# Kernel optimization log

Measured on AMD Instinct MI355X. Metric: run time of the kernel, lower is better.

## Reference

```python
import jax, jax.numpy as jnp
import numpy as np

B, D, NN = 16, 2, 100        # batch, num_depots, num_nodes (pickups+deliveries)
N2 = NN // 2                 # pickups (= deliveries)
NA = D + NN                  # total nodes per batch graph
H, HE, L = 128, 64, 3        # hidden_node_dim, hidden_edge_dim, conv_layers
SLOPE, EPS = 0.2, 1e-5


def _bn(x, g, b):
    # BatchNorm1d in training mode: per-feature batch stats (biased var)
    m = jnp.mean(x, axis=0)
    v = jnp.var(x, axis=0)
    return (x - m) * jax.lax.rsqrt(v + EPS) * g + b


def _leaky(x):
    return jnp.where(x >= 0, x, SLOPE * x)


def _prop(xk, e, m, Wg):
    # Dense-equivalent of GatConv.propagate over a fully-connected per-batch grid.
    # Edge (i, j): x_i = x[target j], x_j = x[source i] (matches edge_index layout:
    # row0 = i repeated, row1 = j blockwise; PyG target = edge_index[1]).
    # xk: [B, N, H] transformed node feats; e: [B, N, N, HE]; m: [B, N, N] 0/1.
    h = xk.shape[-1]
    wi, wj, we = Wg[:h], Wg[h:2 * h], Wg[2 * h:]  # split cat([x_i, x_j, e]) @ Wg
    alpha = _leaky((xk @ wi)[:, None, :, :]        # x_i contribution (target j)
                   + (xk @ wj)[:, :, None, :]      # x_j contribution (source i)
                   + jnp.einsum('bijc,ch->bijh', e, we))
    alpha = jnp.where(m[..., None] != 0, alpha, -jnp.inf)
    alpha = jax.nn.softmax(alpha, axis=1)          # segment softmax keyed by target j
    return jnp.einsum('bijh,bih->bjh', alpha, xk)  # scatter-add x_j * alpha to targets


def _forward(x, demand, time_window, edge_attr_d, edge_attr_r,
             W0, W1, W2, W3, W4,
             b0_g, b0_b, b1_g, b1_b, b2_g, b2_b, b3_g, b3_b, b4_g, b4_b,
             ff_w1, ff_b1, ff_w2, ff_b2, bn_g, bn_b,
             Wvla, Wvlp, Wvld, Wga, Wgp, Wgd,
             edge_index, mask_adjacency_d, mask_adjacency_r):
    ds = jnp.concatenate([x, demand, time_window], axis=-1)  # [B, NA, 5]
    dep = _bn(ds[:, :D].reshape(B * D, -1) @ W0, b0_g, b0_b).reshape(B, D, H)
    pk_in = jnp.concatenate([ds[:, D:D + N2], ds[:, D + N2:D + NN]], axis=-1).reshape(B * N2, -1)
    pk = _bn(pk_in @ W1, b1_g, b1_b).reshape(B, N2, H)
    dl = _bn(ds[:, D + N2:D + NN].reshape(B * N2, -1) @ W2, b2_g, b2_b).reshape(B, N2, H)
    e_d = _bn(edge_attr_d.reshape(-1, edge_attr_d.shape[-1]) @ W3, b3_g, b3_b).reshape(B, NA, NA, HE)
    e_r = _bn(edge_attr_r.reshape(-1, edge_attr_r.shape[-1]) @ W4, b4_g, b4_b).reshape(B, NA, NA, HE)
    m_d = mask_adjacency_d.reshape(B, NA, NA)
    m_r = mask_adjacency_r.reshape(B, NA, NA)

    def conv(xc, e, m, l):
        xall = xc @ Wvla[l]
        pick = xc[:, D:D + N2] @ Wvlp[l]
        deli = xc[:, D + N2:D + NN] @ Wvld[l]
        X1 = _prop(xall, e, m, Wga[l])
        X2 = _prop(pick, e[:, D:D + N2, D:D + N2], m[:, D:D + N2, D:D + N2], Wgp[l])
        X3 = _prop(deli, e[:, D + N2:D + NN, D + N2:D + NN], m[:, D + N2:D + NN, D + N2:D + NN], Wgd[l])
        # faithful to torch.cat(dim=0) followed by view(B, -1, H)
        Xc = jnp.concatenate([X1.reshape(-1, H), X2.reshape(-1, H), X3.reshape(-1, H)], axis=0).reshape(B, -1, H)
        xa, xp, xdd = Xc[:, :NA], Xc[:, NA:NA + N2], Xc[:, NA + N2:NA + NN]
        return jnp.concatenate([xa[:, :D], xa[:, D:D + N2] + xp, xa[:, D + N2:] + xdd], axis=1)

    xd = jnp.concatenate([dep, pk, dl], axis=1)  # [B, NA, H]
    xr = xd
    for l in range(L):
        xd, xr = conv(xd, e_d, m_d, l), conv(xr, e_r, m_r, l)

    def ff_bn(xc):
        xf = xc.reshape(-1, H)
        f = jax.nn.relu(xf @ ff_w1 + ff_b1) @ ff_w2 + ff_b2
        return _bn(xf + f, bn_g, bn_b).reshape(B, NA, H)

    return ff_bn(xd), ff_bn(xr)


def setup_inputs() -> dict:
    key = jax.random.key(0)
    it = iter(jax.random.split(key, 40))

    def nrm(shape, s=0.05):
        return (s * jax.random.normal(next(it), shape)).astype(jnp.float32)

    def uni(shape):
        return jax.random.uniform(next(it), shape, dtype=jnp.float32)

    x = nrm((B, NA, 2), 1.0)
    # first D entries per batch are depots (demand == 0), rest are nonzero
    demand = jnp.concatenate([jnp.zeros((B, D, 1), jnp.float32), uni((B, NN, 1)) + 0.5], axis=1)
    time_window = uni((B, NA, 2))
    edge_attr_d = uni((B, NA * NA, 2))
    edge_attr_r = uni((B, NA * NA, 2))
    eye = jnp.eye(NA, dtype=jnp.int32)[None]
    mask_d = jnp.maximum(jax.random.randint(next(it), (B, NA, NA), 0, 2, dtype=jnp.int32), eye).reshape(B, NA * NA)
    mask_r = jnp.maximum(jax.random.randint(next(it), (B, NA, NA), 0, 2, dtype=jnp.int32), eye).reshape(B, NA * NA)
    ii = jnp.arange(B * NA, dtype=jnp.int32)
    edge_index = jnp.stack([jnp.repeat(ii, NA), jnp.repeat(ii.reshape(B, NA), NA, axis=0).reshape(-1)])

    inp = dict(
        x=x, demand=demand, time_window=time_window,
        edge_attr_d=edge_attr_d, edge_attr_r=edge_attr_r,
        W0=nrm((5, H)), W1=nrm((10, H)), W2=nrm((5, H)), W3=nrm((2, HE)), W4=nrm((2, HE)),
        b0_g=jnp.ones(H, jnp.float32), b0_b=jnp.zeros(H, jnp.float32),
        b1_g=jnp.ones(H, jnp.float32), b1_b=jnp.zeros(H, jnp.float32),
        b2_g=jnp.ones(H, jnp.float32), b2_b=jnp.zeros(H, jnp.float32),
        b3_g=jnp.ones(HE, jnp.float32), b3_b=jnp.zeros(HE, jnp.float32),
        b4_g=jnp.ones(HE, jnp.float32), b4_b=jnp.zeros(HE, jnp.float32),
        ff_w1=nrm((H, H)), ff_b1=jnp.zeros(H, jnp.float32),
        ff_w2=nrm((H, H)), ff_b2=jnp.zeros(H, jnp.float32),
        bn_g=jnp.ones(H, jnp.float32), bn_b=jnp.zeros(H, jnp.float32),
        Wvla=nrm((L, H, H)), Wvlp=nrm((L, H, H)), Wvld=nrm((L, H, H)),
        Wga=nrm((L, 2 * H + HE, H)), Wgp=nrm((L, 2 * H + HE, H)), Wgd=nrm((L, 2 * H + HE, H)),
        edge_index=edge_index, mask_adjacency_d=mask_d, mask_adjacency_r=mask_r,
    )
    return inp


def reference(x, demand, time_window, edge_attr_d, edge_attr_r,
              W0, W1, W2, W3, W4,
              b0_g, b0_b, b1_g, b1_b, b2_g, b2_b, b3_g, b3_b, b4_g, b4_b,
              ff_w1, ff_b1, ff_w2, ff_b2, bn_g, bn_b,
              Wvla, Wvlp, Wvld, Wga, Wgp, Wgd,
              edge_index, mask_adjacency_d, mask_adjacency_r):
    return _forward(x, demand, time_window, edge_attr_d, edge_attr_r,
                    W0, W1, W2, W3, W4,
                    b0_g, b0_b, b1_g, b1_b, b2_g, b2_b, b3_g, b3_b, b4_g, b4_b,
                    ff_w1, ff_b1, ff_w2, ff_b2, bn_g, bn_b,
                    Wvla, Wvlp, Wvld, Wga, Wgp, Wgd,
                    edge_index, mask_adjacency_d, mask_adjacency_r)
```

## Files before the change

kernel.cpp:

```cpp
#include <hip/hip_runtime.h>
#include <stdint.h>

#define B 16
#define D 2
#define NN 100
#define N2 50
#define NA 102
#define H 128
#define HE 64
#define L 3
#define SLOPE 0.2f
#define EPS 1e-5f

#define NAE (NA*NA)
#define EN (B*NAE)
#define R1 (B*NA)
#define R2 (B*N2)
#define RV (R1 + 2*R2)
#define NC 202
#define J 8
#define TI 34

#define MOM_PART  0
#define ACC_NODE  1408
#define ACC_FF    2176
#define OFF_PQR   2816
#define OFF_X0    9728
#define OFF_V     (OFF_X0 + R1*H)
#define OFF_AB    (OFF_V + 2*RV*H)
#define OFF_XO    (OFF_AB + 2*RV*2*H)
#define OFF_Z     (OFF_XO + 2*RV*H)

__device__ __forceinline__ void decode_vrow(int ridx, int& b, int& node) {
    if (ridx < R1) { b = ridx / NA; node = ridx % NA; }
    else if (ridx < R1 + R2) { int p = ridx - R1; b = p / N2; node = D + p % N2; }
    else { int p = ridx - R1 - R2; b = p / N2; node = D + N2 + p % N2; }
}
__device__ __forceinline__ void decode_nrow(int vr, int& b, int& node) {
    if (vr < 32) { b = vr >> 1; node = vr & 1; }
    else if (vr < 832) { int p = vr - 32; b = p / N2; node = D + p % N2; }
    else { int p = vr - 832; b = p / N2; node = D + N2 + p % N2; }
}
__device__ __forceinline__ float combined(const float* __restrict__ XO, int b, int node, int k) {
    float v = XO[(b*NC + node)*H + k];
    if (node >= D) v += XO[(b*NC + node + 100)*H + k];
    return v;
}

__global__ __launch_bounds__(256) void k_moments(const float* __restrict__ ea_d,
                                                 const float* __restrict__ ea_r,
                                                 float* __restrict__ ws) {
    int g = blockIdx.x >> 7;
    int bb = blockIdx.x & 127;
    const float2* ea = (const float2*)(g ? ea_r : ea_d);
    float s0 = 0, s1 = 0, s00 = 0, s11 = 0, s01 = 0;
    for (int idx = bb*256 + threadIdx.x; idx < EN; idx += 128*256) {
        float2 v = ea[idx];
        s0 += v.x; s1 += v.y; s00 += v.x*v.x; s11 += v.y*v.y; s01 += v.x*v.y;
    }
    __shared__ float sd[256];
    float vals[5] = {s0, s1, s00, s11, s01};
    for (int q = 0; q < 5; q++) {
        sd[threadIdx.x] = vals[q];
        __syncthreads();
        for (int off = 128; off > 0; off >>= 1) {
            if (threadIdx.x < off) sd[threadIdx.x] += sd[threadIdx.x + off];
            __syncthreads();
        }
        if (threadIdx.x == 0) ws[MOM_PART + (g*128 + bb)*5 + q] = sd[0];
        __syncthreads();
    }
}

__global__ __launch_bounds__(128) void k_stpqr(const float* __restrict__ W3, const float* __restrict__ W4,
                                               const float* __restrict__ b3g, const float* __restrict__ b3b,
                                               const float* __restrict__ b4g, const float* __restrict__ b4b,
                                               const float* __restrict__ Wga, const float* __restrict__ Wgp,
                                               const float* __restrict__ Wgd, float* __restrict__ ws) {
    int bx = blockIdx.x;
    int g = bx / 9, rem = bx % 9, seg = rem / 3, l = rem % 3;
    int t = threadIdx.x;
    if (bx == 0) {
        for (int i = t; i < 1280; i += 128) ws[ACC_NODE + i] = 0.0f;
    }
    __shared__ float momsh[5];
    __shared__ float st[192];
    if (t < 5) {
        float s = 0;
        for (int p = 0; p < 128; p++) s += ws[MOM_PART + (g*128 + p)*5 + t];
        momsh[t] = s;
    }
    __syncthreads();
    if (t < 64) {
        const float* W  = g ? W4 : W3;
        const float* gv = g ? b4g : b3g;
        const float* bv = g ? b4b : b3b;
        float Nr = (float)EN;
        float S0 = momsh[0], S1 = momsh[1], S00 = momsh[2], S11 = momsh[3], S01 = momsh[4];
        float w0 = W[t], w1 = W[64 + t];
        float m = (S0*w0 + S1*w1) / Nr;
        float E2 = (S00*w0*w0 + 2.0f*S01*w0*w1 + S11*w1*w1) / Nr;
        float var = E2 - m*m;
        float s = gv[t] * rsqrtf(var + EPS);
        st[t] = w0 * s; st[64 + t] = w1 * s; st[128 + t] = bv[t] - m*s;
    }
    __syncthreads();
    int h = t;
    const float* Wg = (seg == 0 ? Wga : (seg == 1 ? Wgp : Wgd)) + l*320*H;
    float P = 0, Q = 0, Rr = 0;
    for (int cc = 0; cc < HE; cc++) {
        float w = Wg[(2*H + cc)*H + h];
        P += st[cc]*w; Q += st[64 + cc]*w; Rr += st[128 + cc]*w;
    }
    float* o = ws + OFF_PQR + ((g*3 + seg)*3 + l)*384;
    o[h] = P; o[128 + h] = Q; o[256 + h] = Rr;
}

__global__ __launch_bounds__(128) void k_nodeinit(const float* __restrict__ x, const float* __restrict__ dm,
                                                  const float* __restrict__ tw,
                                                  const float* __restrict__ W0, const float* __restrict__ W1,
                                                  const float* __restrict__ W2, float* __restrict__ ws) {
    int c = threadIdx.x, bx = blockIdx.x;
    int seg = (bx < 2) ? 0 : (bx < 52 ? 1 : 2);
    const float* W = seg == 0 ? W0 : (seg == 1 ? W1 : W2);
    int nf = seg == 1 ? 10 : 5;
    float w[10];
    for (int f = 0; f < nf; f++) w[f] = W[f*H + c];
    float* x0 = ws + OFF_X0;
    float ls = 0, lss = 0;
    for (int r = 0; r < 16; r++) {
        int vr = bx*16 + r;
        int b, node; decode_nrow(vr, b, node);
        int row = b*NA + node;
        float y = x[row*2]*w[0] + x[row*2+1]*w[1] + dm[row]*w[2]
                + tw[row*2]*w[3] + tw[row*2+1]*w[4];
        if (seg == 1) {
            int r2 = row + N2;
            y += x[r2*2]*w[5] + x[r2*2+1]*w[6] + dm[r2]*w[7]
               + tw[r2*2]*w[8] + tw[r2*2+1]*w[9];
        }
        x0[row*H + c] = y;
        ls += y; lss += y*y;
    }
    atomicAdd(&ws[ACC_NODE + seg*256 + c], ls);
    atomicAdd(&ws[ACC_NODE + seg*256 + 128 + c], lss);
}

__global__ __launch_bounds__(128) void k_nodenorm(const float* __restrict__ b0g, const float* __restrict__ b0b,
                                                  const float* __restrict__ b1g, const float* __restrict__ b1b,
                                                  const float* __restrict__ b2g, const float* __restrict__ b2b,
                                                  float* __restrict__ ws) {
    int c = threadIdx.x, bx = blockIdx.x;
    int seg = (bx < 2) ? 0 : (bx < 52 ? 1 : 2);
    float cnt = seg == 0 ? 32.0f : 800.0f;
    float m = ws[ACC_NODE + seg*256 + c] / cnt;
    float v = ws[ACC_NODE + seg*256 + 128 + c] / cnt - m*m;
    const float* gp = seg == 0 ? b0g : (seg == 1 ? b1g : b2g);
    const float* bp = seg == 0 ? b0b : (seg == 1 ? b1b : b2b);
    float sc = gp[c] * rsqrtf(v + EPS);
    float sh = bp[c] - m*sc;
    float* x0 = ws + OFF_X0;
    for (int r = 0; r < 16; r++) {
        int vr = bx*16 + r;
        int b, node; decode_nrow(vr, b, node);
        int row = b*NA + node;
        x0[row*H + c] = x0[row*H + c]*sc + sh;
    }
}

__global__ __launch_bounds__(256) void k_gemmVA(const float* __restrict__ Wvla, const float* __restrict__ Wvlp,
                                                const float* __restrict__ Wvld,
                                                const float* __restrict__ Wga, const float* __restrict__ Wgp,
                                                const float* __restrict__ Wgd,
                                                int layer, float* __restrict__ ws) {
    __shared__ float xs[8][H];
    __shared__ float vs[8][H];
    int g = blockIdx.x / 404, tb = blockIdx.x % 404;
    int rowbase = tb * 8;
    const float* x0 = ws + OFF_X0;
    const float* XO = ws + OFF_XO + g*RV*H;
    for (int e = 0; e < 4; e++) {
        int lin = threadIdx.x + e*256;
        int r = lin >> 7, k = lin & 127;
        int b, node; decode_vrow(rowbase + r, b, node);
        xs[r][k] = (layer == 0) ? x0[(b*NA + node)*H + k] : combined(XO, b, node, k);
    }
    __syncthreads();
    int seg = tb < 204 ? 0 : (tb < 304 ? 1 : 2);
    const float* W = (seg == 0 ? Wvla : (seg == 1 ? Wvlp : Wvld)) + layer*H*H;
    int col = threadIdx.x & 127, half = threadIdx.x >> 7;
    float acc[4] = {0,0,0,0};
    const float* Wp = W + col;
    float w0 = Wp[0], w1 = Wp[H], w2 = Wp[2*H], w3 = Wp[3*H];
    for (int k4 = 0; k4 < 32; k4++) {
        int kn = ((k4 + 1) & 31) * 4;
        const float* q = Wp + kn*H;
        float n0 = q[0], n1 = q[H], n2 = q[2*H], n3 = q[3*H];
        #pragma unroll
        for (int rr = 0; rr < 4; rr++) {
            float4 x4 = *(const float4*)&xs[half + rr*2][4*k4];
            acc[rr] = fmaf(x4.w, w3, fmaf(x4.z, w2, fmaf(x4.y, w1, fmaf(x4.x, w0, acc[rr]))));
        }
        w0 = n0; w1 = n1; w2 = n2; w3 = n3;
    }
    float* V = ws + OFF_V + g*RV*H;
    #pragma unroll
    for (int rr = 0; rr < 4; rr++) {
        vs[half + rr*2][col] = acc[rr];
        V[(rowbase + half + rr*2)*H + col] = acc[rr];
    }
    __syncthreads();
    const float* Wg = (seg == 0 ? Wga : (seg == 1 ? Wgp : Wgd)) + layer*320*H;
    int c = threadIdx.x;
    const float* wb = Wg + ((c >> 7) * H) * H + (c & 127);
    float a2[8];
    #pragma unroll
    for (int rr = 0; rr < 8; rr++) a2[rr] = 0.0f;
    float v0 = wb[0], v1 = wb[H], v2 = wb[2*H], v3 = wb[3*H];
    for (int k4 = 0; k4 < 32; k4++) {
        int kn = ((k4 + 1) & 31) * 4;
        const float* q = wb + kn*H;
        float n0 = q[0], n1 = q[H], n2 = q[2*H], n3 = q[3*H];
        #pragma unroll
        for (int rr = 0; rr < 8; rr++) {
            float4 x4 = *(const float4*)&vs[rr][4*k4];
            a2[rr] = fmaf(x4.w, v3, fmaf(x4.z, v2, fmaf(x4.y, v1, fmaf(x4.x, v0, a2[rr]))));
        }
        v0 = n0; v1 = n1; v2 = n2; v3 = n3;
    }
    float* AB = ws + OFF_AB + g*RV*2*H;
    #pragma unroll
    for (int rr = 0; rr < 8; rr++) AB[(rowbase + rr)*256 + c] = a2[rr];
}

__global__ __launch_bounds__(512) void k_attn(const float* __restrict__ ea_d, const float* __restrict__ ea_r,
                                              const int* __restrict__ mask_d, const int* __restrict__ mask_r,
                                              int layer, float* __restrict__ ws) {
    int k = blockIdx.x, y = blockIdx.y;
    int ci = y / 27, r = y % 27;
    int combo = k + 8*ci;
    int g = combo >> 4, b = combo & 15;
    int seg, jg, n, o, base;
    if (r < 13)      { seg = 0; jg = r;      n = NA; o = 0;      base = 0; }
    else if (r < 20) { seg = 1; jg = r - 13; n = N2; o = D;      base = R1; }
    else             { seg = 2; jg = r - 20; n = N2; o = D + N2; base = R1 + R2; }
    int j0 = jg * J;
    int jc = min(J, n - j0);
    int tid = threadIdx.x;
    int c = tid & 63, wv = tid >> 6;
    int pair = wv & 3, ihalf = wv >> 2;
    int jj0 = 2*pair, jj1 = 2*pair + 1;

    const float* pqr = ws + OFF_PQR + ((g*3 + seg)*3 + layer)*384;
    float2 Pv = ((const float2*)pqr)[c];
    float2 Qv = ((const float2*)(pqr + 128))[c];
    float2 Rv = ((const float2*)(pqr + 256))[c];
    const float2* ea = (const float2*)(g ? ea_r : ea_d);
    const int* mask = g ? mask_r : mask_d;
    const float* V  = ws + OFF_V  + g*RV*H   + base*H;
    const float* AB = ws + OFF_AB + g*RV*2*H + base*2*H;

    __shared__ float2 Bs[TI][64];
    __shared__ float2 Vs[TI][64];
    __shared__ float2 se[J][104];
    __shared__ int    msk_s[104];

    if (tid < n) {
        int ibase = b*NAE + (o + tid)*NA + o + j0;
        int bits = 0;
        #pragma unroll
        for (int jj = 0; jj < J; jj++) {
            int valid = (jj < jc) ? (mask[ibase + jj] != 0) : 0;
            bits |= valid << jj;
            se[jj][tid] = valid ? ea[ibase + jj] : make_float2(0.f, 0.f);
        }
        msk_s[tid] = bits;
    }

    float2 Aj0 = make_float2(0.f, 0.f), Aj1 = make_float2(0.f, 0.f);
    if (jj0 < jc) Aj0 = *(const float2*)&AB[(b*n + j0 + jj0)*256 + 2*c];
    if (jj1 < jc) Aj1 = *(const float2*)&AB[(b*n + j0 + jj1)*256 + 2*c];
    float A0x = Aj0.x + Rv.x, A0y = Aj0.y + Rv.y;
    float A1x = Aj1.x + Rv.x, A1y = Aj1.y + Rv.y;
    float2 l0 = make_float2(0.f, 0.f), a0 = make_float2(0.f, 0.f);
    float2 l1 = make_float2(0.f, 0.f), a1 = make_float2(0.f, 0.f);

    int nh = (n + 1) >> 1;
    int i0w = ihalf ? nh : 0;
    int i1w = ihalf ? n : nh;

    for (int t0 = 0; t0 < n; t0 += TI) {
        int rows = min(TI, n - t0);
        __syncthreads();
        for (int idx = tid; idx < rows*64; idx += 512) {
            int ir = idx >> 6, cc = idx & 63;
            int gi = b*n + t0 + ir;
            Bs[ir][cc] = *(const float2*)&AB[gi*256 + 128 + 2*cc];
            Vs[ir][cc] = *(const float2*)&V[gi*128 + 2*cc];
        }
        __syncthreads();
        int irlo = max(0, i0w - t0);
        int irhi = min(rows, i1w - t0);
        for (int ir = irlo; ir < irhi; ir++) {
            int i = t0 + ir;
            int bits = msk_s[i];
            if (!(bits & ((1<<jj0) | (1<<jj1)))) continue;
            float2 Bi = Bs[ir][c];
            float2 Vi = Vs[ir][c];
            if (bits & (1<<jj0)) {
                float2 ev = se[jj0][i];
                float tx = fmaf(ev.x, Pv.x, fmaf(ev.y, Qv.x, A0x + Bi.x));
                float ty = fmaf(ev.x, Pv.y, fmaf(ev.y, Qv.y, A0y + Bi.y));
                tx = fminf(fmaxf(tx, SLOPE*tx), 80.0f);
                ty = fminf(fmaxf(ty, SLOPE*ty), 80.0f);
                float px = __expf(tx), py = __expf(ty);
                l0.x += px; l0.y += py;
                a0.x = fmaf(px, Vi.x, a0.x); a0.y = fmaf(py, Vi.y, a0.y);
            }
            if (bits & (1<<jj1)) {
                float2 ev = se[jj1][i];
                float tx = fmaf(ev.x, Pv.x, fmaf(ev.y, Qv.x, A1x + Bi.x));
                float ty = fmaf(ev.x, Pv.y, fmaf(ev.y, Qv.y, A1y + Bi.y));
                tx = fminf(fmaxf(tx, SLOPE*tx), 80.0f);
                ty = fminf(fmaxf(ty, SLOPE*ty), 80.0f);
                float px = __expf(tx), py = __expf(ty);
                l1.x += px; l1.y += py;
                a1.x = fmaf(px, Vi.x, a1.x); a1.y = fmaf(py, Vi.y, a1.y);
            }
        }
    }
    __syncthreads();
    float* mg = (float*)Bs;
    if (ihalf == 1) {
        mg[(0*4 + pair)*64 + c] = l0.x;  mg[(1*4 + pair)*64 + c] = l0.y;
        mg[(2*4 + pair)*64 + c] = l1.x;  mg[(3*4 + pair)*64 + c] = l1.y;
        mg[(4*4 + pair)*64 + c] = a0.x;  mg[(5*4 + pair)*64 + c] = a0.y;
        mg[(6*4 + pair)*64 + c] = a1.x;  mg[(7*4 + pair)*64 + c] = a1.y;
    }
    __syncthreads();
    if (ihalf == 0) {
        l0.x += mg[(0*4 + pair)*64 + c];  l0.y += mg[(1*4 + pair)*64 + c];
        l1.x += mg[(2*4 + pair)*64 + c];  l1.y += mg[(3*4 + pair)*64 + c];
        a0.x += mg[(4*4 + pair)*64 + c];  a0.y += mg[(5*4 + pair)*64 + c];
        a1.x += mg[(6*4 + pair)*64 + c];  a1.y += mg[(7*4 + pair)*64 + c];
        float* XO = ws + OFF_XO + g*RV*H + base*H;
        if (jj0 < jc)
            ((float2*)&XO[(b*n + j0 + jj0)*H])[c] = make_float2(a0.x/l0.x, a0.y/l0.y);
        if (jj1 < jc)
            ((float2*)&XO[(b*n + j0 + jj1)*H])[c] = make_float2(a1.x/l1.x, a1.y/l1.y);
    }
}

__global__ __launch_bounds__(256) void k_ff(const float* __restrict__ ffw1, const float* __restrict__ ffb1,
                                            const float* __restrict__ ffw2, const float* __restrict__ ffb2,
                                            float* __restrict__ ws) {
    __shared__ float xs[8][H];
    __shared__ float hs[8][H];
    int g = blockIdx.x / 204, tb = blockIdx.x % 204;
    int rowbase = tb * 8;
    const float* XO = ws + OFF_XO + g*RV*H;
    for (int e = 0; e < 4; e++) {
        int lin = threadIdx.x + e*256;
        int r = lin >> 7, k = lin & 127;
        int ridx = rowbase + r;
        int b = ridx / NA, node = ridx % NA;
        xs[r][k] = combined(XO, b, node, k);
    }
    __syncthreads();
    int col = threadIdx.x & 127, half = threadIdx.x >> 7;
    float acc[4] = {0,0,0,0};
    const float* W1p = ffw1 + col;
    float w0 = W1p[0], w1 = W1p[H], w2 = W1p[2*H], w3 = W1p[3*H];
    for (int k4 = 0; k4 < 32; k4++) {
        int kn = ((k4 + 1) & 31) * 4;
        const float* q = W1p + kn*H;
        float n0 = q[0], n1 = q[H], n2 = q[2*H], n3 = q[3*H];
        #pragma unroll
        for (int rr = 0; rr < 4; rr++) {
            float4 x4 = *(const float4*)&xs[half + rr*2][4*k4];
            acc[rr] = fmaf(x4.w, w3, fmaf(x4.z, w2, fmaf(x4.y, w1, fmaf(x4.x, w0, acc[rr]))));
        }
        w0 = n0; w1 = n1; w2 = n2; w3 = n3;
    }
    float b1 = ffb1[col];
    #pragma unroll
    for (int rr = 0; rr < 4; rr++) {
        float hv = acc[rr] + b1;
        hs[half + rr*2][col] = hv > 0.0f ? hv : 0.0f;
    }
    __syncthreads();
    #pragma unroll
    for (int rr = 0; rr < 4; rr++) acc[rr] = 0.0f;
    const float* W2p = ffw2 + col;
    w0 = W2p[0]; w1 = W2p[H]; w2 = W2p[2*H]; w3 = W2p[3*H];
    for (int k4 = 0; k4 < 32; k4++) {
        int kn = ((k4 + 1) & 31) * 4;
        const float* q = W2p + kn*H;
        float n0 = q[0], n1 = q[H], n2 = q[2*H], n3 = q[3*H];
        #pragma unroll
        for (int rr = 0; rr < 4; rr++) {
            float4 x4 = *(const float4*)&hs[half + rr*2][4*k4];
            acc[rr] = fmaf(x4.w, w3, fmaf(x4.z, w2, fmaf(x4.y, w1, fmaf(x4.x, w0, acc[rr]))));
        }
        w0 = n0; w1 = n1; w2 = n2; w3 = n3;
    }
    float b2 = ffb2[col];
    float* Z = ws + OFF_Z + g*R1*H;
    float ls = 0, lss = 0;
    #pragma unroll
    for (int rr = 0; rr < 4; rr++) {
        int row = rowbase + half + rr*2;
        float z = acc[rr] + b2 + xs[half + rr*2][col];
        Z[row*H + col] = z;
        ls += z; lss += z*z;
    }
    atomicAdd(&ws[ACC_FF + g*256 + col], ls);
    atomicAdd(&ws[ACC_FF + g*256 + 128 + col], lss);
}

__global__ __launch_bounds__(256) void k_f3(const float* __restrict__ bng, const float* __restrict__ bnb,
                                            float* __restrict__ ws, float* __restrict__ out) {
    int eidx = blockIdx.x * 256 + threadIdx.x;
    int g = eidx / (R1*H);
    int c = eidx & 127;
    float m = ws[ACC_FF + g*256 + c] / 1632.0f;
    float v = ws[ACC_FF + g*256 + 128 + c] / 1632.0f - m*m;
    float sc = bng[c] * rsqrtf(v + EPS);
    float sh = bnb[c] - m*sc;
    out[eidx] = ws[OFF_Z + eidx] * sc + sh;
}

extern "C" void kernel_launch(void* const* d_in, const int* in_sizes, int n_in,
                              void* d_out, int out_size, void* d_ws, size_t ws_size,
                              hipStream_t stream) {
    const float* x    = (const float*)d_in[0];
    const float* dm   = (const float*)d_in[1];
    const float* tw   = (const float*)d_in[2];
    const float* ead  = (const float*)d_in[3];
    const float* ear  = (const float*)d_in[4];
    const float* W0   = (const float*)d_in[5];
    const float* W1   = (const float*)d_in[6];
    const float* W2   = (const float*)d_in[7];
    const float* W3   = (const float*)d_in[8];
    const float* W4   = (const float*)d_in[9];
    const float* b0g  = (const float*)d_in[10];
    const float* b0b  = (const float*)d_in[11];
    const float* b1g  = (const float*)d_in[12];
    const float* b1b  = (const float*)d_in[13];
    const float* b2g  = (const float*)d_in[14];
    const float* b2b  = (const float*)d_in[15];
    const float* b3g  = (const float*)d_in[16];
    const float* b3b  = (const float*)d_in[17];
    const float* b4g  = (const float*)d_in[18];
    const float* b4b  = (const float*)d_in[19];
    const float* ffw1 = (const float*)d_in[20];
    const float* ffb1 = (const float*)d_in[21];
    const float* ffw2 = (const float*)d_in[22];
    const float* ffb2 = (const float*)d_in[23];
    const float* bng  = (const float*)d_in[24];
    const float* bnb  = (const float*)d_in[25];
    const float* Wvla = (const float*)d_in[26];
    const float* Wvlp = (const float*)d_in[27];
    const float* Wvld = (const float*)d_in[28];
    const float* Wga  = (const float*)d_in[29];
    const float* Wgp  = (const float*)d_in[30];
    const float* Wgd  = (const float*)d_in[31];
    const int* mask_d = (const int*)d_in[33];
    const int* mask_r = (const int*)d_in[34];
    float* ws = (float*)d_ws;
    float* out = (float*)d_out;

    k_moments <<<256, 256, 0, stream>>>(ead, ear, ws);
    k_stpqr   <<<18, 128, 0, stream>>>(W3, W4, b3g, b3b, b4g, b4b, Wga, Wgp, Wgd, ws);
    k_nodeinit<<<102, 128, 0, stream>>>(x, dm, tw, W0, W1, W2, ws);
    k_nodenorm<<<102, 128, 0, stream>>>(b0g, b0b, b1g, b1b, b2g, b2b, ws);
    for (int l = 0; l < L; l++) {
        k_gemmVA<<<808, 256, 0, stream>>>(Wvla, Wvlp, Wvld, Wga, Wgp, Wgd, l, ws);
        k_attn  <<<dim3(8, 108), 512, 0, stream>>>(ead, ear, mask_d, mask_r, l, ws);
    }
    k_ff<<<408, 256, 0, stream>>>(ffw1, ffb1, ffw2, ffb2, ws);
    k_f3<<<1632, 256, 0, stream>>>(bng, bnb, ws, out);
}
```

Before: 327.4 us.

## Merge all stages into one persistent cooperative kernel with grid syncs

Replaces the chain of separate launches with a single cooperative persistent kernel whose phases are separated by grid-wide barriers, with a multi-launch fallback. Node BN statistics move from atomics to per-block partials, and the attention phase drops from 512 to 256 threads (tile size changed). The goal is to remove per-launch overhead and gaps between the many small kernels. In exchange it risks lower occupancy from the large shared buffer and launch bounds, grid-sync costs, and less parallelism in the attention stage.

```diff
diff --git a/kernel.cpp b/kernel.cpp
--- a/kernel.cpp
+++ b/kernel.cpp
@@ -1,5 +1,7 @@
 #include <hip/hip_runtime.h>
+#include <hip/hip_cooperative_groups.h>
 #include <stdint.h>
+namespace cg = cooperative_groups;
 
 #define B 16
 #define D 2
@@ -18,19 +20,30 @@
 #define R2 (B*N2)
 #define RV (R1 + 2*R2)
 #define NC 202
-#define J 8
-#define TI 34
+#define TI 26
 
 #define MOM_PART  0
-#define ACC_NODE  1408
-#define ACC_FF    2176
-#define OFF_PQR   2816
-#define OFF_X0    9728
+#define NODE_PART 1280
+#define ACC_FF    27392
+#define OFF_PQR   27904
+#define OFF_X0    34816
 #define OFF_V     (OFF_X0 + R1*H)
 #define OFF_AB    (OFF_V + 2*RV*H)
 #define OFF_XO    (OFF_AB + 2*RV*2*H)
 #define OFF_Z     (OFF_XO + 2*RV*H)
 
+#define SMEM_FLOATS 8704
+
+struct KParams {
+    const float *x, *dm, *tw, *ead, *ear;
+    const float *W0, *W1, *W2, *W3, *W4;
+    const float *b0g, *b0b, *b1g, *b1b, *b2g, *b2b, *b3g, *b3b, *b4g, *b4b;
+    const float *ffw1, *ffb1, *ffw2, *ffb2, *bng, *bnb;
+    const float *Wvla, *Wvlp, *Wvld, *Wga, *Wgp, *Wgd;
+    const int *mask_d, *mask_r;
+    float *ws, *out;
+};
+
 __device__ __forceinline__ void decode_vrow(int ridx, int& b, int& node) {
     if (ridx < R1) { b = ridx / NA; node = ridx % NA; }
     else if (ridx < R1 + R2) { int p = ridx - R1; b = p / N2; node = D + p % N2; }
@@ -47,148 +60,142 @@
     return v;
 }
 
-__global__ __launch_bounds__(256) void k_moments(const float* __restrict__ ea_d,
-                                                 const float* __restrict__ ea_r,
-                                                 float* __restrict__ ws) {
-    int g = blockIdx.x >> 7;
-    int bb = blockIdx.x & 127;
-    const float2* ea = (const float2*)(g ? ea_r : ea_d);
+
+__device__ void phase_moments(int u, int tid, float* smem, const KParams& p) {
+    int g = u >> 7, bb = u & 127;
+    const float2* ea = (const float2*)(g ? p.ear : p.ead);
     float s0 = 0, s1 = 0, s00 = 0, s11 = 0, s01 = 0;
-    for (int idx = bb*256 + threadIdx.x; idx < EN; idx += 128*256) {
+    for (int idx = bb*256 + tid; idx < EN; idx += 128*256) {
         float2 v = ea[idx];
         s0 += v.x; s1 += v.y; s00 += v.x*v.x; s11 += v.y*v.y; s01 += v.x*v.y;
     }
-    __shared__ float sd[256];
     float vals[5] = {s0, s1, s00, s11, s01};
     for (int q = 0; q < 5; q++) {
-        sd[threadIdx.x] = vals[q];
+        smem[tid] = vals[q];
         __syncthreads();
         for (int off = 128; off > 0; off >>= 1) {
-            if (threadIdx.x < off) sd[threadIdx.x] += sd[threadIdx.x + off];
+            if (tid < off) smem[tid] += smem[tid + off];
             __syncthreads();
         }
-        if (threadIdx.x == 0) ws[MOM_PART + (g*128 + bb)*5 + q] = sd[0];
-        __syncthreads();
-    }
-}
-
-__global__ __launch_bounds__(128) void k_stpqr(const float* __restrict__ W3, const float* __restrict__ W4,
-                                               const float* __restrict__ b3g, const float* __restrict__ b3b,
-                                               const float* __restrict__ b4g, const float* __restrict__ b4b,
-                                               const float* __restrict__ Wga, const float* __restrict__ Wgp,
-                                               const float* __restrict__ Wgd, float* __restrict__ ws) {
-    int bx = blockIdx.x;
-    int g = bx / 9, rem = bx % 9, seg = rem / 3, l = rem % 3;
-    int t = threadIdx.x;
-    if (bx == 0) {
-        for (int i = t; i < 1280; i += 128) ws[ACC_NODE + i] = 0.0f;
-    }
-    __shared__ float momsh[5];
-    __shared__ float st[192];
-    if (t < 5) {
+        if (tid == 0) p.ws[MOM_PART + (g*128 + bb)*5 + q] = smem[0];
+        __syncthreads();
+    }
+}
+
+__device__ void phase_nodeinit(int u, int tid, const KParams& p) {
+    int half = tid >> 7, c = tid & 127;
+    int vb = u*2 + half;
+    int seg = (vb < 2) ? 0 : (vb < 52 ? 1 : 2);
+    const float* W = seg == 0 ? p.W0 : (seg == 1 ? p.W1 : p.W2);
+    int nf = seg == 1 ? 10 : 5;
+    float w[10];
+    for (int f = 0; f < nf; f++) w[f] = W[f*H + c];
+    float* x0 = p.ws + OFF_X0;
+    float ls = 0, lss = 0;
+    for (int r = 0; r < 16; r++) {
+        int vr = vb*16 + r;
+        int b, node; decode_nrow(vr, b, node);
+        int row = b*NA + node;
+        float y = p.x[row*2]*w[0] + p.x[row*2+1]*w[1] + p.dm[row]*w[2]
+                + p.tw[row*2]*w[3] + p.tw[row*2+1]*w[4];
+        if (seg == 1) {
+            int r2 = row + N2;
+            y += p.x[r2*2]*w[5] + p.x[r2*2+1]*w[6] + p.dm[r2]*w[7]
+               + p.tw[r2*2]*w[8] + p.tw[r2*2+1]*w[9];
+        }
+        x0[row*H + c] = y;
+        ls += y; lss += y*y;
+    }
+    p.ws[NODE_PART + vb*256 + c] = ls;
+    p.ws[NODE_PART + vb*256 + 128 + c] = lss;
+}
+
+__device__ void phase_zero(int tid, const KParams& p) {
+    for (int i = tid; i < 512; i += 256) p.ws[ACC_FF + i] = 0.0f;
+}
+
+__device__ void phase_stpqr(int u, int tid, float* smem, const KParams& p) {
+    int g = u / 9, rem = u % 9, seg = rem / 3, lay = rem % 3;
+    float* st = smem;
+    float* momsh = smem + 256;
+    if (tid < 5) {
         float s = 0;
-        for (int p = 0; p < 128; p++) s += ws[MOM_PART + (g*128 + p)*5 + t];
-        momsh[t] = s;
-    }
-    __syncthreads();
-    if (t < 64) {
-        const float* W  = g ? W4 : W3;
-        const float* gv = g ? b4g : b3g;
-        const float* bv = g ? b4b : b3b;
+        for (int q = 0; q < 128; q++) s += p.ws[MOM_PART + (g*128 + q)*5 + tid];
+        momsh[tid] = s;
+    }
+    __syncthreads();
+    if (tid < 64) {
+        const float* W  = g ? p.W4 : p.W3;
+        const float* gv = g ? p.b4g : p.b3g;
+        const float* bv = g ? p.b4b : p.b3b;
         float Nr = (float)EN;
         float S0 = momsh[0], S1 = momsh[1], S00 = momsh[2], S11 = momsh[3], S01 = momsh[4];
-        float w0 = W[t], w1 = W[64 + t];
+        float w0 = W[tid], w1 = W[64 + tid];
         float m = (S0*w0 + S1*w1) / Nr;
         float E2 = (S00*w0*w0 + 2.0f*S01*w0*w1 + S11*w1*w1) / Nr;
         float var = E2 - m*m;
-        float s = gv[t] * rsqrtf(var + EPS);
-        st[t] = w0 * s; st[64 + t] = w1 * s; st[128 + t] = bv[t] - m*s;
-    }
-    __syncthreads();
-    int h = t;
-    const float* Wg = (seg == 0 ? Wga : (seg == 1 ? Wgp : Wgd)) + l*320*H;
-    float P = 0, Q = 0, Rr = 0;
-    for (int cc = 0; cc < HE; cc++) {
-        float w = Wg[(2*H + cc)*H + h];
-        P += st[cc]*w; Q += st[64 + cc]*w; Rr += st[128 + cc]*w;
-    }
-    float* o = ws + OFF_PQR + ((g*3 + seg)*3 + l)*384;
-    o[h] = P; o[128 + h] = Q; o[256 + h] = Rr;
-}
-
-__global__ __launch_bounds__(128) void k_nodeinit(const float* __restrict__ x, const float* __restrict__ dm,
-                                                  const float* __restrict__ tw,
-                                                  const float* __restrict__ W0, const float* __restrict__ W1,
-                                                  const float* __restrict__ W2, float* __restrict__ ws) {
-    int c = threadIdx.x, bx = blockIdx.x;
-    int seg = (bx < 2) ? 0 : (bx < 52 ? 1 : 2);
-    const float* W = seg == 0 ? W0 : (seg == 1 ? W1 : W2);
-    int nf = seg == 1 ? 10 : 5;
-    float w[10];
-    for (int f = 0; f < nf; f++) w[f] = W[f*H + c];
-    float* x0 = ws + OFF_X0;
-    float ls = 0, lss = 0;
-    for (int r = 0; r < 16; r++) {
-        int vr = bx*16 + r;
-        int b, node; decode_nrow(vr, b, node);
-        int row = b*NA + node;
-        float y = x[row*2]*w[0] + x[row*2+1]*w[1] + dm[row]*w[2]
-                + tw[row*2]*w[3] + tw[row*2+1]*w[4];
-        if (seg == 1) {
-            int r2 = row + N2;
-            y += x[r2*2]*w[5] + x[r2*2+1]*w[6] + dm[r2]*w[7]
-               + tw[r2*2]*w[8] + tw[r2*2+1]*w[9];
-        }
-        x0[row*H + c] = y;
-        ls += y; lss += y*y;
-    }
-    atomicAdd(&ws[ACC_NODE + seg*256 + c], ls);
-    atomicAdd(&ws[ACC_NODE + seg*256 + 128 + c], lss);
-}
-
-__global__ __launch_bounds__(128) void k_nodenorm(const float* __restrict__ b0g, const float* __restrict__ b0b,
-                                                  const float* __restrict__ b1g, const float* __restrict__ b1b,
-                                                  const float* __restrict__ b2g, const float* __restrict__ b2b,
-                                                  float* __restrict__ ws) {
-    int c = threadIdx.x, bx = blockIdx.x;
-    int seg = (bx < 2) ? 0 : (bx < 52 ? 1 : 2);
-    float cnt = seg == 0 ? 32.0f : 800.0f;
-    float m = ws[ACC_NODE + seg*256 + c] / cnt;
-    float v = ws[ACC_NODE + seg*256 + 128 + c] / cnt - m*m;
-    const float* gp = seg == 0 ? b0g : (seg == 1 ? b1g : b2g);
-    const float* bp = seg == 0 ? b0b : (seg == 1 ? b1b : b2b);
-    float sc = gp[c] * rsqrtf(v + EPS);
-    float sh = bp[c] - m*sc;
-    float* x0 = ws + OFF_X0;
-    for (int r = 0; r < 16; r++) {
-        int vr = bx*16 + r;
-        int b, node; decode_nrow(vr, b, node);
-        int row = b*NA + node;
-        x0[row*H + c] = x0[row*H + c]*sc + sh;
-    }
-}
-
-__global__ __launch_bounds__(256) void k_gemmVA(const float* __restrict__ Wvla, const float* __restrict__ Wvlp,
-                                                const float* __restrict__ Wvld,
-                                                const float* __restrict__ Wga, const float* __restrict__ Wgp,
-                                                const float* __restrict__ Wgd,
-                                                int layer, float* __restrict__ ws) {
-    __shared__ float xs[8][H];
-    __shared__ float vs[8][H];
-    int g = blockIdx.x / 404, tb = blockIdx.x % 404;
+        float s = gv[tid] * rsqrtf(var + EPS);
+        st[tid] = w0 * s; st[64 + tid] = w1 * s; st[128 + tid] = bv[tid] - m*s;
+    }
+    __syncthreads();
+    if (tid < 128) {
+        int h = tid;
+        const float* Wg = (seg == 0 ? p.Wga : (seg == 1 ? p.Wgp : p.Wgd)) + lay*320*H;
+        float P = 0, Q = 0, Rr = 0;
+        for (int cc = 0; cc < HE; cc++) {
+            float w = Wg[(2*H + cc)*H + h];
+            P += st[cc]*w; Q += st[64 + cc]*w; Rr += st[128 + cc]*w;
+        }
+        float* o = p.ws + OFF_PQR + ((g*3 + seg)*3 + lay)*384;
+        o[h] = P; o[128 + h] = Q; o[256 + h] = Rr;
+    }
+    __syncthreads();
+}
+
+__device__ void phase_nodenorm(int vb, int tid, const KParams& p) {
+    if (tid < 128) {
+        int c = tid;
+        int seg = (vb < 2) ? 0 : (vb < 52 ? 1 : 2);
+        int lo = seg == 0 ? 0 : (seg == 1 ? 2 : 52);
+        int hi = seg == 0 ? 2 : (seg == 1 ? 52 : 102);
+        float s = 0, ss = 0;
+        for (int q = lo; q < hi; q++) {
+            s  += p.ws[NODE_PART + q*256 + c];
+            ss += p.ws[NODE_PART + q*256 + 128 + c];
+        }
+        float cnt = seg == 0 ? 32.0f : 800.0f;
+        float m = s / cnt, v = ss / cnt - m*m;
+        const float* gp = seg == 0 ? p.b0g : (seg == 1 ? p.b1g : p.b2g);
+        const float* bp = seg == 0 ? p.b0b : (seg == 1 ? p.b1b : p.b2b);
+        float sc = gp[c] * rsqrtf(v + EPS);
+        float sh = bp[c] - m*sc;
+        float* x0 = p.ws + OFF_X0;
+        for (int r = 0; r < 16; r++) {
+            int vr = vb*16 + r;
+            int b, node; decode_nrow(vr, b, node);
+            int row = b*NA + node;
+            x0[row*H + c] = x0[row*H + c]*sc + sh;
+        }
+    }
+}
+
+__device__ void phase_gemm(int u, int lay, int tid, float* smem, const KParams& p) {
+    float* xs = smem;
+    float* vs = smem + 1024;
+    int g = u / 404, tb = u % 404;
     int rowbase = tb * 8;
-    const float* x0 = ws + OFF_X0;
-    const float* XO = ws + OFF_XO + g*RV*H;
+    const float* x0 = p.ws + OFF_X0;
+    const float* XO = p.ws + OFF_XO + g*RV*H;
     for (int e = 0; e < 4; e++) {
-        int lin = threadIdx.x + e*256;
+        int lin = tid + e*256;
         int r = lin >> 7, k = lin & 127;
         int b, node; decode_vrow(rowbase + r, b, node);
-        xs[r][k] = (layer == 0) ? x0[(b*NA + node)*H + k] : combined(XO, b, node, k);
+        xs[r*H + k] = (lay == 0) ? x0[(b*NA + node)*H + k] : combined(XO, b, node, k);
     }
     __syncthreads();
     int seg = tb < 204 ? 0 : (tb < 304 ? 1 : 2);
-    const float* W = (seg == 0 ? Wvla : (seg == 1 ? Wvlp : Wvld)) + layer*H*H;
-    int col = threadIdx.x & 127, half = threadIdx.x >> 7;
+    const float* W = (seg == 0 ? p.Wvla : (seg == 1 ? p.Wvlp : p.Wvld)) + lay*H*H;
+    int col = tid & 127, half = tid >> 7;
     float acc[4] = {0,0,0,0};
     const float* Wp = W + col;
     float w0 = Wp[0], w1 = Wp[H], w2 = Wp[2*H], w3 = Wp[3*H];
@@ -198,21 +205,20 @@
         float n0 = q[0], n1 = q[H], n2 = q[2*H], n3 = q[3*H];
         #pragma unroll
         for (int rr = 0; rr < 4; rr++) {
-            float4 x4 = *(const float4*)&xs[half + rr*2][4*k4];
+            float4 x4 = *(const float4*)&xs[(half + rr*2)*H + 4*k4];
             acc[rr] = fmaf(x4.w, w3, fmaf(x4.z, w2, fmaf(x4.y, w1, fmaf(x4.x, w0, acc[rr]))));
         }
         w0 = n0; w1 = n1; w2 = n2; w3 = n3;
     }
-    float* V = ws + OFF_V + g*RV*H;
+    float* V = p.ws + OFF_V + g*RV*H;
     #pragma unroll
     for (int rr = 0; rr < 4; rr++) {
-        vs[half + rr*2][col] = acc[rr];
+        vs[(half + rr*2)*H + col] = acc[rr];
         V[(rowbase + half + rr*2)*H + col] = acc[rr];
     }
     __syncthreads();
-    const float* Wg = (seg == 0 ? Wga : (seg == 1 ? Wgp : Wgd)) + layer*320*H;
-    int c = threadIdx.x;
-    const float* wb = Wg + ((c >> 7) * H) * H + (c & 127);
+    const float* Wg = (seg == 0 ? p.Wga : (seg == 1 ? p.Wgp : p.Wgd)) + lay*320*H;
+    const float* wb = Wg + ((tid >> 7) * H) * H + (tid & 127);
     float a2[8];
     #pragma unroll
     for (int rr = 0; rr < 8; rr++) a2[rr] = 0.0f;
@@ -223,58 +229,54 @@
         float n0 = q[0], n1 = q[H], n2 = q[2*H], n3 = q[3*H];
         #pragma unroll
         for (int rr = 0; rr < 8; rr++) {
-            float4 x4 = *(const float4*)&vs[rr][4*k4];
+            float4 x4 = *(const float4*)&vs[rr*H + 4*k4];
             a2[rr] = fmaf(x4.w, v3, fmaf(x4.z, v2, fmaf(x4.y, v1, fmaf(x4.x, v0, a2[rr]))));
         }
         v0 = n0; v1 = n1; v2 = n2; v3 = n3;
     }
-    float* AB = ws + OFF_AB + g*RV*2*H;
+    float* AB = p.ws + OFF_AB + g*RV*2*H;
     #pragma unroll
-    for (int rr = 0; rr < 8; rr++) AB[(rowbase + rr)*256 + c] = a2[rr];
-}
-
-__global__ __launch_bounds__(512) void k_attn(const float* __restrict__ ea_d, const float* __restrict__ ea_r,
-                                              const int* __restrict__ mask_d, const int* __restrict__ mask_r,
-                                              int layer, float* __restrict__ ws) {
-    int k = blockIdx.x, y = blockIdx.y;
+    for (int rr = 0; rr < 8; rr++) AB[(rowbase + rr)*256 + tid] = a2[rr];
+}
+
+__device__ void phase_attn(int u, int lay, int tid, float* smem, const KParams& p) {
+    int kx = u & 7, y = u >> 3;
     int ci = y / 27, r = y % 27;
-    int combo = k + 8*ci;
+    int combo = kx + 8*ci;
     int g = combo >> 4, b = combo & 15;
     int seg, jg, n, o, base;
     if (r < 13)      { seg = 0; jg = r;      n = NA; o = 0;      base = 0; }
     else if (r < 20) { seg = 1; jg = r - 13; n = N2; o = D;      base = R1; }
     else             { seg = 2; jg = r - 20; n = N2; o = D + N2; base = R1 + R2; }
-    int j0 = jg * J;
-    int jc = min(J, n - j0);
-    int tid = threadIdx.x;
+    int j0 = jg * 8;
+    int jc = min(8, n - j0);
     int c = tid & 63, wv = tid >> 6;
-    int pair = wv & 3, ihalf = wv >> 2;
-    int jj0 = 2*pair, jj1 = 2*pair + 1;
-
-    const float* pqr = ws + OFF_PQR + ((g*3 + seg)*3 + layer)*384;
+    int jj0 = 2*wv, jj1 = jj0 + 1;
+
+    const float* pqr = p.ws + OFF_PQR + ((g*3 + seg)*3 + lay)*384;
     float2 Pv = ((const float2*)pqr)[c];
     float2 Qv = ((const float2*)(pqr + 128))[c];
     float2 Rv = ((const float2*)(pqr + 256))[c];
-    const float2* ea = (const float2*)(g ? ea_r : ea_d);
-    const int* mask = g ? mask_r : mask_d;
-    const float* V  = ws + OFF_V  + g*RV*H   + base*H;
-    const float* AB = ws + OFF_AB + g*RV*2*H + base*2*H;
-
-    __shared__ float2 Bs[TI][64];
-    __shared__ float2 Vs[TI][64];
-    __shared__ float2 se[J][104];
-    __shared__ int    msk_s[104];
+    const float2* ea = (const float2*)(g ? p.ear : p.ead);
+    const int* mask = g ? p.mask_r : p.mask_d;
+    const float* V  = p.ws + OFF_V  + g*RV*H   + base*H;
+    const float* AB = p.ws + OFF_AB + g*RV*2*H + base*2*H;
+
+    float2* Bs = (float2*)smem;
+    float2* Vs = (float2*)(smem + 2*TI*64);
+    float2* se = (float2*)(smem + 4*TI*64);
+    int*   msk = (int*)(smem + 4*TI*64 + 1664);
 
     if (tid < n) {
         int ibase = b*NAE + (o + tid)*NA + o + j0;
         int bits = 0;
         #pragma unroll
-        for (int jj = 0; jj < J; jj++) {
+        for (int jj = 0; jj < 8; jj++) {
             int valid = (jj < jc) ? (mask[ibase + jj] != 0) : 0;
             bits |= valid << jj;
-            se[jj][tid] = valid ? ea[ibase + jj] : make_float2(0.f, 0.f);
-        }
-        msk_s[tid] = bits;
+            se[jj*104 + tid] = valid ? ea[ibase + jj] : make_float2(0.f, 0.f);
+        }
+        msk[tid] = bits;
     }
 
     float2 Aj0 = make_float2(0.f, 0.f), Aj1 = make_float2(0.f, 0.f);
@@ -285,30 +287,24 @@
     float2 l0 = make_float2(0.f, 0.f), a0 = make_float2(0.f, 0.f);
     float2 l1 = make_float2(0.f, 0.f), a1 = make_float2(0.f, 0.f);
 
-    int nh = (n + 1) >> 1;
-    int i0w = ihalf ? nh : 0;
-    int i1w = ihalf ? n : nh;
-
     for (int t0 = 0; t0 < n; t0 += TI) {
         int rows = min(TI, n - t0);
         __syncthreads();
-        for (int idx = tid; idx < rows*64; idx += 512) {
+        for (int idx = tid; idx < rows*64; idx += 256) {
             int ir = idx >> 6, cc = idx & 63;
             int gi = b*n + t0 + ir;
-            Bs[ir][cc] = *(const float2*)&AB[gi*256 + 128 + 2*cc];
-            Vs[ir][cc] = *(const float2*)&V[gi*128 + 2*cc];
-        }
-        __syncthreads();
-        int irlo = max(0, i0w - t0);
-        int irhi = min(rows, i1w - t0);
-        for (int ir = irlo; ir < irhi; ir++) {
+            Bs[ir*64 + cc] = *(const float2*)&AB[gi*256 + 128 + 2*cc];
+            Vs[ir*64 + cc] = *(const float2*)&V[gi*128 + 2*cc];
+        }
+        __syncthreads();
+        for (int ir = 0; ir < rows; ir++) {
             int i = t0 + ir;
-            int bits = msk_s[i];
+            int bits = msk[i];
             if (!(bits & ((1<<jj0) | (1<<jj1)))) continue;
-            float2 Bi = Bs[ir][c];
-            float2 Vi = Vs[ir][c];
+            float2 Bi = Bs[ir*64 + c];
+            float2 Vi = Vs[ir*64 + c];
             if (bits & (1<<jj0)) {
-                float2 ev = se[jj0][i];
+                float2 ev = se[jj0*104 + i];
                 float tx = fmaf(ev.x, Pv.x, fmaf(ev.y, Qv.x, A0x + Bi.x));
                 float ty = fmaf(ev.x, Pv.y, fmaf(ev.y, Qv.y, A0y + Bi.y));
                 tx = fminf(fmaxf(tx, SLOPE*tx), 80.0f);
@@ -318,7 +314,7 @@
                 a0.x = fmaf(px, Vi.x, a0.x); a0.y = fmaf(py, Vi.y, a0.y);
             }
             if (bits & (1<<jj1)) {
-                float2 ev = se[jj1][i];
+                float2 ev = se[jj1*104 + i];
                 float tx = fmaf(ev.x, Pv.x, fmaf(ev.y, Qv.x, A1x + Bi.x));
                 float ty = fmaf(ev.x, Pv.y, fmaf(ev.y, Qv.y, A1y + Bi.y));
                 tx = fminf(fmaxf(tx, SLOPE*tx), 80.0f);
@@ -329,47 +325,31 @@
             }
         }
     }
-    __syncthreads();
-    float* mg = (float*)Bs;
-    if (ihalf == 1) {
-        mg[(0*4 + pair)*64 + c] = l0.x;  mg[(1*4 + pair)*64 + c] = l0.y;
-        mg[(2*4 + pair)*64 + c] = l1.x;  mg[(3*4 + pair)*64 + c] = l1.y;
-        mg[(4*4 + pair)*64 + c] = a0.x;  mg[(5*4 + pair)*64 + c] = a0.y;
-        mg[(6*4 + pair)*64 + c] = a1.x;  mg[(7*4 + pair)*64 + c] = a1.y;
-    }
-    __syncthreads();
-    if (ihalf == 0) {
-        l0.x += mg[(0*4 + pair)*64 + c];  l0.y += mg[(1*4 + pair)*64 + c];
-        l1.x += mg[(2*4 + pair)*64 + c];  l1.y += mg[(3*4 + pair)*64 + c];
-        a0.x += mg[(4*4 + pair)*64 + c];  a0.y += mg[(5*4 + pair)*64 + c];
-        a1.x += mg[(6*4 + pair)*64 + c];  a1.y += mg[(7*4 + pair)*64 + c];
-        float* XO = ws + OFF_XO + g*RV*H + base*H;
-        if (jj0 < jc)
-            ((float2*)&XO[(b*n + j0 + jj0)*H])[c] = make_float2(a0.x/l0.x, a0.y/l0.y);
-        if (jj1 < jc)
-            ((float2*)&XO[(b*n + j0 + jj1)*H])[c] = make_float2(a1.x/l1.x, a1.y/l1.y);
-    }
-}
-
-__global__ __launch_bounds__(256) void k_ff(const float* __restrict__ ffw1, const float* __restrict__ ffb1,
-                                            const float* __restrict__ ffw2, const float* __restrict__ ffb2,
-                                            float* __restrict__ ws) {
-    __shared__ float xs[8][H];
-    __shared__ float hs[8][H];
-    int g = blockIdx.x / 204, tb = blockIdx.x % 204;
+    float* XO = p.ws + OFF_XO + g*RV*H + base*H;
+    if (jj0 < jc)
+        ((float2*)&XO[(b*n + j0 + jj0)*H])[c] = make_float2(a0.x/l0.x, a0.y/l0.y);
+    if (jj1 < jc)
+        ((float2*)&XO[(b*n + j0 + jj1)*H])[c] = make_float2(a1.x/l1.x, a1.y/l1.y);
+    __syncthreads();
+}
+
+__device__ void phase_ff(int u, int tid, float* smem, const KParams& p) {
+    float* xs = smem;
+    float* hs = smem + 1024;
+    int g = u / 204, tb = u % 204;
     int rowbase = tb * 8;
-    const float* XO = ws + OFF_XO + g*RV*H;
+    const float* XO = p.ws + OFF_XO + g*RV*H;
     for (int e = 0; e < 4; e++) {
-        int lin = threadIdx.x + e*256;
+        int lin = tid + e*256;
         int r = lin >> 7, k = lin & 127;
         int ridx = rowbase + r;
         int b = ridx / NA, node = ridx % NA;
-        xs[r][k] = combined(XO, b, node, k);
-    }
-    __syncthreads();
-    int col = threadIdx.x & 127, half = threadIdx.x >> 7;
+        xs[r*H + k] = combined(XO, b, node, k);
+    }
+    __syncthreads();
+    int col = tid & 127, half = tid >> 7;
     float acc[4] = {0,0,0,0};
-    const float* W1p = ffw1 + col;
+    const float* W1p = p.ffw1 + col;
     float w0 = W1p[0], w1 = W1p[H], w2 = W1p[2*H], w3 = W1p[3*H];
     for (int k4 = 0; k4 < 32; k4++) {
         int kn = ((k4 + 1) & 31) * 4;
@@ -377,21 +357,21 @@
         float n0 = q[0], n1 = q[H], n2 = q[2*H], n3 = q[3*H];
         #pragma unroll
         for (int rr = 0; rr < 4; rr++) {
-            float4 x4 = *(const float4*)&xs[half + rr*2][4*k4];
+            float4 x4 = *(const float4*)&xs[(half + rr*2)*H + 4*k4];
             acc[rr] = fmaf(x4.w, w3, fmaf(x4.z, w2, fmaf(x4.y, w1, fmaf(x4.x, w0, acc[rr]))));
         }
         w0 = n0; w1 = n1; w2 = n2; w3 = n3;
     }
-    float b1 = ffb1[col];
+    float b1 = p.ffb1[col];
     #pragma unroll
     for (int rr = 0; rr < 4; rr++) {
         float hv = acc[rr] + b1;
-        hs[half + rr*2][col] = hv > 0.0f ? hv : 0.0f;
+        hs[(half + rr*2)*H + col] = hv > 0.0f ? hv : 0.0f;
     }
     __syncthreads();
     #pragma unroll
     for (int rr = 0; rr < 4; rr++) acc[rr] = 0.0f;
-    const float* W2p = ffw2 + col;
+    const float* W2p = p.ffw2 + col;
     w0 = W2p[0]; w1 = W2p[H]; w2 = W2p[2*H]; w3 = W2p[3*H];
     for (int k4 = 0; k4 < 32; k4++) {
         int kn = ((k4 + 1) & 31) * 4;
@@ -399,85 +379,167 @@
         float n0 = q[0], n1 = q[H], n2 = q[2*H], n3 = q[3*H];
         #pragma unroll
         for (int rr = 0; rr < 4; rr++) {
-            float4 x4 = *(const float4*)&hs[half + rr*2][4*k4];
+            float4 x4 = *(const float4*)&hs[(half + rr*2)*H + 4*k4];
             acc[rr] = fmaf(x4.w, w3, fmaf(x4.z, w2, fmaf(x4.y, w1, fmaf(x4.x, w0, acc[rr]))));
         }
         w0 = n0; w1 = n1; w2 = n2; w3 = n3;
     }
-    float b2 = ffb2[col];
-    float* Z = ws + OFF_Z + g*R1*H;
+    float b2 = p.ffb2[col];
+    float* Z = p.ws + OFF_Z + g*R1*H;
     float ls = 0, lss = 0;
     #pragma unroll
     for (int rr = 0; rr < 4; rr++) {
         int row = rowbase + half + rr*2;
-        float z = acc[rr] + b2 + xs[half + rr*2][col];
+        float z = acc[rr] + b2 + xs[(half + rr*2)*H + col];
         Z[row*H + col] = z;
         ls += z; lss += z*z;
     }
-    atomicAdd(&ws[ACC_FF + g*256 + col], ls);
-    atomicAdd(&ws[ACC_FF + g*256 + 128 + col], lss);
-}
-
-__global__ __launch_bounds__(256) void k_f3(const float* __restrict__ bng, const float* __restrict__ bnb,
-                                            float* __restrict__ ws, float* __restrict__ out) {
-    int eidx = blockIdx.x * 256 + threadIdx.x;
-    int g = eidx / (R1*H);
-    int c = eidx & 127;
-    float m = ws[ACC_FF + g*256 + c] / 1632.0f;
-    float v = ws[ACC_FF + g*256 + 128 + c] / 1632.0f - m*m;
-    float sc = bng[c] * rsqrtf(v + EPS);
-    float sh = bnb[c] - m*sc;
-    out[eidx] = ws[OFF_Z + eidx] * sc + sh;
+    atomicAdd(&p.ws[ACC_FF + g*256 + col], ls);
+    atomicAdd(&p.ws[ACC_FF + g*256 + 128 + col], lss);
+    __syncthreads();
+}
+
+__device__ __forceinline__ void phase_f3(int e, const KParams& p) {
+    int g = e / (R1*H);
+    int c = e & 127;
+    float m = p.ws[ACC_FF + g*256 + c] / 1632.0f;
+    float v = p.ws[ACC_FF + g*256 + 128 + c] / 1632.0f - m*m;
+    float sc = p.bng[c] * rsqrtf(v + EPS);
+    float sh = p.bnb[c] - m*sc;
+    p.out[e] = p.ws[OFF_Z + e] * sc + sh;
+}
+
+__global__ __launch_bounds__(256, 4) void k_all(KParams p) {
+    cg::grid_group gg = cg::this_grid();
+    __shared__ float smem[SMEM_FLOATS];
+    int bid = blockIdx.x, tid = threadIdx.x, nb = gridDim.x;
+
+    for (int u = bid; u < 308; u += nb) {
+        __syncthreads();
+        if (u < 256) phase_moments(u, tid, smem, p);
+        else if (u < 307) phase_nodeinit(u - 256, tid, p);
+        else phase_zero(tid, p);
+    }
+    gg.sync();
+    for (int u = bid; u < 120; u += nb) {
+        __syncthreads();
+        if (u < 18) phase_stpqr(u, tid, smem, p);
+        else phase_nodenorm(u - 18, tid, p);
+    }
+    gg.sync();
+    for (int lay = 0; lay < L; lay++) {
+        for (int u = bid; u < 808; u += nb) {
+            __syncthreads();
+            phase_gemm(u, lay, tid, smem, p);
+        }
+        gg.sync();
+        for (int u = bid; u < 864; u += nb) {
+            __syncthreads();
+            phase_attn(u, lay, tid, smem, p);
+        }
+        gg.sync();
+    }
+    for (int u = bid; u < 408; u += nb) {
+        __syncthreads();
+        phase_ff(u, tid, smem, p);
+    }
+    gg.sync();
+    for (int e = bid*256 + tid; e < 2*R1*H; e += nb*256) phase_f3(e, p);
+}
+
+__global__ __launch_bounds__(256) void kf_A(KParams p) {
+    __shared__ float smem[SMEM_FLOATS];
+    int u = blockIdx.x, tid = threadIdx.x;
+    if (u < 256) phase_moments(u, tid, smem, p);
+    else if (u < 307) phase_nodeinit(u - 256, tid, p);
+    else phase_zero(tid, p);
+}
+__global__ __launch_bounds__(256) void kf_B(KParams p) {
+    __shared__ float smem[SMEM_FLOATS];
+    int u = blockIdx.x, tid = threadIdx.x;
+    if (u < 18) phase_stpqr(u, tid, smem, p);
+    else phase_nodenorm(u - 18, tid, p);
+}
+__global__ __launch_bounds__(256) void kf_gemm(KParams p, int lay) {
+    __shared__ float smem[SMEM_FLOATS];
+    phase_gemm(blockIdx.x, lay, threadIdx.x, smem, p);
+}
+__global__ __launch_bounds__(256) void kf_attn(KParams p, int lay) {
+    __shared__ float smem[SMEM_FLOATS];
+    phase_attn(blockIdx.x, lay, threadIdx.x, smem, p);
+}
+__global__ __launch_bounds__(256) void kf_ff(KParams p) {
+    __shared__ float smem[SMEM_FLOATS];
+    phase_ff(blockIdx.x, threadIdx.x, smem, p);
+}
+__global__ __launch_bounds__(256) void kf_f3(KParams p) {
+    int e = blockIdx.x * 256 + threadIdx.x;
+    if (e < 2*R1*H) phase_f3(e, p);
 }
 
 extern "C" void kernel_launch(void* const* d_in, const int* in_sizes, int n_in,
                               void* d_out, int out_size, void* d_ws, size_t ws_size,
                               hipStream_t stream) {
-    const float* x    = (const float*)d_in[0];
-    const float* dm   = (const float*)d_in[1];
-    const float* tw   = (const float*)d_in[2];
-    const float* ead  = (const float*)d_in[3];
-    const float* ear  = (const float*)d_in[4];
-    const float* W0   = (const float*)d_in[5];
-    const float* W1   = (const float*)d_in[6];
-    const float* W2   = (const float*)d_in[7];
-    const float* W3   = (const float*)d_in[8];
-    const float* W4   = (const float*)d_in[9];
-    const float* b0g  = (const float*)d_in[10];
-    const float* b0b  = (const float*)d_in[11];
-    const float* b1g  = (const float*)d_in[12];
-    const float* b1b  = (const float*)d_in[13];
-    const float* b2g  = (const float*)d_in[14];
-    const float* b2b  = (const float*)d_in[15];
-    const float* b3g  = (const float*)d_in[16];
-    const float* b3b  = (const float*)d_in[17];
-    const float* b4g  = (const float*)d_in[18];
-    const float* b4b  = (const float*)d_in[19];
-    const float* ffw1 = (const float*)d_in[20];
-    const float* ffb1 = (const float*)d_in[21];
-    const float* ffw2 = (const float*)d_in[22];
-    const float* ffb2 = (const float*)d_in[23];
-    const float* bng  = (const float*)d_in[24];
-    const float* bnb  = (const float*)d_in[25];
-    const float* Wvla = (const float*)d_in[26];
-    const float* Wvlp = (const float*)d_in[27];
-    const float* Wvld = (const float*)d_in[28];
-    const float* Wga  = (const float*)d_in[29];
-    const float* Wgp  = (const float*)d_in[30];
-    const float* Wgd  = (const float*)d_in[31];
-    const int* mask_d = (const int*)d_in[33];
-    const int* mask_r = (const int*)d_in[34];
-    float* ws = (float*)d_ws;
-    float* out = (float*)d_out;
-
-    k_moments <<<256, 256, 0, stream>>>(ead, ear, ws);
-    k_stpqr   <<<18, 128, 0, stream>>>(W3, W4, b3g, b3b, b4g, b4b, Wga, Wgp, Wgd, ws);
-    k_nodeinit<<<102, 128, 0, stream>>>(x, dm, tw, W0, W1, W2, ws);
-    k_nodenorm<<<102, 128, 0, stream>>>(b0g, b0b, b1g, b1b, b2g, b2b, ws);
-    for (int l = 0; l < L; l++) {
-        k_gemmVA<<<808, 256, 0, stream>>>(Wvla, Wvlp, Wvld, Wga, Wgp, Wgd, l, ws);
-        k_attn  <<<dim3(8, 108), 512, 0, stream>>>(ead, ear, mask_d, mask_r, l, ws);
-    }
-    k_ff<<<408, 256, 0, stream>>>(ffw1, ffb1, ffw2, ffb2, ws);
-    k_f3<<<1632, 256, 0, stream>>>(bng, bnb, ws, out);
-}
+    KParams p;
+    p.x    = (const float*)d_in[0];
+    p.dm   = (const float*)d_in[1];
+    p.tw   = (const float*)d_in[2];
+    p.ead  = (const float*)d_in[3];
+    p.ear  = (const float*)d_in[4];
+    p.W0   = (const float*)d_in[5];
+    p.W1   = (const float*)d_in[6];
+    p.W2   = (const float*)d_in[7];
+    p.W3   = (const float*)d_in[8];
+    p.W4   = (const float*)d_in[9];
+    p.b0g  = (const float*)d_in[10];
+    p.b0b  = (const float*)d_in[11];
+    p.b1g  = (const float*)d_in[12];
+    p.b1b  = (const float*)d_in[13];
+    p.b2g  = (const float*)d_in[14];
+    p.b2b  = (const float*)d_in[15];
+    p.b3g  = (const float*)d_in[16];
+    p.b3b  = (const float*)d_in[17];
+    p.b4g  = (const float*)d_in[18];
+    p.b4b  = (const float*)d_in[19];
+    p.ffw1 = (const float*)d_in[20];
+    p.ffb1 = (const float*)d_in[21];
+    p.ffw2 = (const float*)d_in[22];
+    p.ffb2 = (const float*)d_in[23];
+    p.bng  = (const float*)d_in[24];
+    p.bnb  = (const float*)d_in[25];
+    p.Wvla = (const float*)d_in[26];
+    p.Wvlp = (const float*)d_in[27];
+    p.Wvld = (const float*)d_in[28];
+    p.Wga  = (const float*)d_in[29];
+    p.Wgp  = (const float*)d_in[30];
+    p.Wgd  = (const float*)d_in[31];
+    p.mask_d = (const int*)d_in[33];
+    p.mask_r = (const int*)d_in[34];
+    p.ws  = (float*)d_ws;
+    p.out = (float*)d_out;
+
+    int dev = 0, cus = 0, maxActive = 0;
+    hipGetDevice(&dev);
+    hipDeviceGetAttribute(&cus, hipDeviceAttributeMultiprocessorCount, dev);
+    hipError_t qerr = hipOccupancyMaxActiveBlocksPerMultiprocessor(&maxActive, k_all, 256, 0);
+    int nb = 0;
+    if (qerr == hipSuccess && cus > 0 && maxActive > 0) {
+        long cap = (long)maxActive * (long)cus;
+        nb = (int)(cap < 864 ? cap : 864);
+    }
+    hipError_t err = hipErrorUnknown;
+    if (nb >= 64) {
+        void* args[] = { &p };
+        err = hipLaunchCooperativeKernel(k_all, dim3(nb), dim3(256), args, 0, stream);
+    }
+    if (err != hipSuccess) {
+        kf_A<<<308, 256, 0, stream>>>(p);
+        kf_B<<<120, 256, 0, stream>>>(p);
+        for (int lay = 0; lay < L; lay++) {
+            kf_gemm<<<808, 256, 0, stream>>>(p, lay);
+            kf_attn<<<864, 256, 0, stream>>>(p, lay);
+        }
+        kf_ff<<<408, 256, 0, stream>>>(p);
+        kf_f3<<<1632, 256, 0, stream>>>(p);
+    }
+}
```

Result: slower. 1.113 ms (+239.9%).
